# Kernel tuning notes

Hardware: AMD Instinct MI355X
Metric: run time of the kernel (lower is better)

Reference implementation:

```python
import jax, jax.numpy as jnp
import numpy as np

BETA = 0.25
N_EMBED = 1024
DIM = 256


def setup_inputs() -> dict:
    key = jax.random.key(0)
    k1, k2 = jax.random.split(key)
    z = jax.random.normal(k1, (8, DIM, 64, 64), dtype=jnp.float32)
    # matches nn.Embedding init: uniform(-1/n_embed, 1/n_embed)
    codebook = jax.random.uniform(
        k2, (N_EMBED, DIM), dtype=jnp.float32,
        minval=-1.0 / N_EMBED, maxval=1.0 / N_EMBED)
    return {"z": z, "codebook": codebook}


def reference(z, codebook):
    B, C, H, W = z.shape
    sg = jax.lax.stop_gradient
    zp = jnp.transpose(z, (0, 2, 3, 1))          # [B,H,W,C]
    zf = zp.reshape(-1, C)                        # [N,C], N = B*H*W
    # squared euclidean distances: ||z||^2 + ||e||^2 - 2 z.e
    d = (jnp.sum(zf * zf, axis=1, keepdims=True)
         + jnp.sum(codebook * codebook, axis=1)
         - 2.0 * zf @ codebook.T)                 # [N, n_embed]
    idx = jnp.argmin(d, axis=1)                   # [N]
    # one-hot @ codebook in the original is just an index gather
    z_q = codebook[idx].reshape(zp.shape)         # [B,H,W,C]
    loss = (BETA * jnp.mean((sg(z_q) - zp) ** 2)
            + jnp.mean((z_q - sg(zp)) ** 2))
    z_q_st = zp + sg(z_q - zp)                    # straight-through estimator
    z_q_out = jnp.transpose(z_q_st, (0, 3, 1, 2))  # back to NCHW
    return z_q_out, loss, idx.reshape(B, H, W)
```

## Files before the change

kernel.cpp:

```cpp
#include <hip/hip_runtime.h>
#include <hip/hip_fp16.h>

#define NELEM 8388608
#define M_GAP 6e-4f
#define SCORE_SCALE (-1.0f / 512.0f)

typedef _Float16 f16x8 __attribute__((ext_vector_type(8)));
typedef short s16x8 __attribute__((ext_vector_type(8)));
typedef float f32x4 __attribute__((ext_vector_type(4)));

__device__ __forceinline__ unsigned short bf16r(float f) {
  unsigned u = __float_as_uint(f);
  return (unsigned short)((u + 0x7fffu + ((u >> 16) & 1u)) >> 16);
}
__device__ __forceinline__ float bf16f(unsigned short h) {
  return __uint_as_float(((unsigned)h) << 16);
}

__device__ __forceinline__ float pw128_sq(const float* p, int s) {
  float r[8];
#pragma unroll
  for (int j = 0; j < 8; ++j) { float v = p[j * s]; r[j] = __fmul_rn(v, v); }
#pragma unroll
  for (int i = 8; i < 128; i += 8) {
#pragma unroll
    for (int j = 0; j < 8; ++j) {
      float v = p[(i + j) * s];
      r[j] = __fadd_rn(r[j], __fmul_rn(v, v));
    }
  }
  return __fadd_rn(__fadd_rn(__fadd_rn(r[0], r[1]), __fadd_rn(r[2], r[3])),
                   __fadd_rn(__fadd_rn(r[4], r[5]), __fadd_rn(r[6], r[7])));
}
__device__ __forceinline__ float np_sumsq256(const float* p, int s) {
  return __fadd_rn(pw128_sq(p, s), pw128_sq(p + 128 * s, s));
}

__global__ __launch_bounds__(256)
void vq_prep(const float* __restrict__ cb, unsigned short* __restrict__ cbimg,
             float* __restrict__ cbT, float* __restrict__ Bsg,
             unsigned* __restrict__ cnt, float* __restrict__ loss) {
  int gid = blockIdx.x * 256 + threadIdx.x;
  if (gid == 0) { *cnt = 0u; *loss = 0.0f; }
  int j = gid >> 2, qt = gid & 3;
  const float4* row4 = reinterpret_cast<const float4*>(cb + (size_t)j * 256 + qt * 64);
  int jt = j >> 5, jj = j & 31;
  unsigned short* baseh = cbimg + (size_t)jt * 8192 + jj * 256;
  int sw = jj << 3;
#pragma unroll
  for (int m = 0; m < 8; ++m) {
    int c0 = qt * 64 + m * 8;
    float4 va = row4[m * 2];
    float4 vb = row4[m * 2 + 1];
    float v[8] = {va.x, va.y, va.z, va.w, vb.x, vb.y, vb.z, vb.w};
    s16x8 hv;
#pragma unroll
    for (int q = 0; q < 8; ++q) {
      hv[q] = (short)__half_as_ushort(__float2half(v[q] * 1024.0f));
      cbT[(size_t)(c0 + q) * 1024 + j] = v[q];
    }
    *reinterpret_cast<s16x8*>(baseh + (c0 ^ sw)) = hv;
  }
  if (qt == 0) Bsg[j] = np_sumsq256(cb + (size_t)j * 256, 1);
}

__global__ __launch_bounds__(256, 4)
void vq_fast(const float* __restrict__ z, const float* __restrict__ cb,
             const unsigned short* __restrict__ cbimg,
             const float* __restrict__ Bsg,
             float* __restrict__ zq, float* __restrict__ loss,
             float* __restrict__ idxo,
             unsigned* __restrict__ list, unsigned* __restrict__ cnt,
             float* __restrict__ zdump) {
  __shared__ __align__(16) unsigned char buf[34816];
  __shared__ float BsL[1024];
  __shared__ float part[32][36];
  __shared__ float rowA[64];
  __shared__ int bestj[64];
  __shared__ float bestd[64];
  __shared__ unsigned char flg[64];
  __shared__ float wred[4];

  const int t = threadIdx.x;
  const int bid = blockIdx.x;
  const int lane = t & 63;
  const int wv = t >> 6;
  const int l15 = lane & 15;
  const int lk = lane >> 4;

  float* zt = reinterpret_cast<float*>(buf);
  const float4* z4 = reinterpret_cast<const float4*>(
      z + (size_t)(bid >> 6) * 1048576 + (size_t)(bid & 63) * 64);

  f16x8 ah[8];
  for (int hp = 0; hp < 2; ++hp) {
    float sq[4] = {0.f, 0.f, 0.f, 0.f};
#pragma unroll
    for (int i = 0; i < 8; ++i) {
      int idx = t + i * 256;
      int c = idx >> 3, w4p = idx & 7;
      float4 v = z4[(size_t)c * 1024 + hp * 8 + w4p];
      zt[c * 33 + w4p * 4 + 0] = v.x;
      zt[c * 33 + w4p * 4 + 1] = v.y;
      zt[c * 33 + w4p * 4 + 2] = v.z;
      zt[c * 33 + w4p * 4 + 3] = v.w;
      sq[0] += v.x * v.x; sq[1] += v.y * v.y;
      sq[2] += v.z * v.z; sq[3] += v.w * v.w;
    }
#pragma unroll
    for (int q = 0; q < 4; ++q) part[t >> 3][(t & 7) * 4 + q] = sq[q];
    __syncthreads();
    if (t < 32) {
      float s = 0.f;
#pragma unroll
      for (int g = 0; g < 32; ++g) s += part[g][t];
      rowA[hp * 32 + t] = s;
    }
    if ((wv >> 1) == hp) {
      int lr = (wv & 1) * 16 + l15;
#pragma unroll
      for (int kk = 0; kk < 8; ++kk)
#pragma unroll
        for (int m = 0; m < 8; ++m)
          ah[kk][m] = (_Float16)zt[(kk * 32 + lk * 8 + m) * 33 + lr];
    }
    if (zdump) {
#pragma unroll
      for (int i = 0; i < 8; ++i) {
        int item = t + i * 256;
        int c4 = item & 63, rowp = item >> 6;
        float4 v = make_float4(zt[(c4 * 4 + 0) * 33 + rowp],
                               zt[(c4 * 4 + 1) * 33 + rowp],
                               zt[(c4 * 4 + 2) * 33 + rowp],
                               zt[(c4 * 4 + 3) * 33 + rowp]);
        *reinterpret_cast<float4*>(
            zdump + ((size_t)bid * 64 + hp * 32 + rowp) * 256 + c4 * 4) = v;
      }
    }
    __syncthreads();
  }

#pragma unroll
  for (int i = 0; i < 4; ++i) {
    int item = t + i * 256;
    *reinterpret_cast<s16x8*>(buf + item * 16) =
        *reinterpret_cast<const s16x8*>((const unsigned char*)cbimg + item * 16);
  }
  for (int i = t; i < 1024; i += 256) BsL[i] = Bsg[i];
  __syncthreads();

  float b1v[2][4], b2v[2][4];
  int b1i[2][4];
#pragma unroll
  for (int js = 0; js < 2; ++js)
#pragma unroll
    for (int r = 0; r < 4; ++r) { b1v[js][r] = 3.4e38f; b2v[js][r] = 3.4e38f; b1i[js][r] = 0; }

  for (int jt = 0; jt < 32; ++jt) {
    const unsigned short* bufH = reinterpret_cast<const unsigned short*>(buf + (jt & 1) * 16384);
    unsigned char* nbuf = buf + ((jt + 1) & 1) * 16384;
    const unsigned char* nsrc = (const unsigned char*)cbimg + (size_t)(jt + 1) * 16384;

    f32x4 acc[2];
    acc[0] = (f32x4){0.f, 0.f, 0.f, 0.f};
    acc[1] = (f32x4){0.f, 0.f, 0.f, 0.f};

    s16x8 g0, g1, g2, g3;
#pragma unroll
    for (int kk = 0; kk < 8; ++kk) {
      if (jt < 31 && kk == 0) {
        g0 = *reinterpret_cast<const s16x8*>(nsrc + (t + 0) * 16);
        g1 = *reinterpret_cast<const s16x8*>(nsrc + (t + 256) * 16);
        g2 = *reinterpret_cast<const s16x8*>(nsrc + (t + 512) * 16);
        g3 = *reinterpret_cast<const s16x8*>(nsrc + (t + 768) * 16);
      }
#pragma unroll
      for (int js = 0; js < 2; ++js) {
        int jj = js * 16 + l15;
        int e = jj * 256 + ((kk * 32 + lk * 8) ^ (jj << 3));
        f16x8 bh = *reinterpret_cast<const f16x8*>(bufH + e);
        acc[js] = __builtin_amdgcn_mfma_f32_16x16x32_f16(ah[kk], bh, acc[js], 0, 0, 0);
      }
      if (jt < 31 && kk == 4) {
        *reinterpret_cast<s16x8*>(nbuf + (t + 0) * 16) = g0;
        *reinterpret_cast<s16x8*>(nbuf + (t + 256) * 16) = g1;
        *reinterpret_cast<s16x8*>(nbuf + (t + 512) * 16) = g2;
        *reinterpret_cast<s16x8*>(nbuf + (t + 768) * 16) = g3;
      }
    }

#pragma unroll
    for (int js = 0; js < 2; ++js) {
      int j = jt * 32 + js * 16 + l15;
      float Bj = BsL[j];
#pragma unroll
      for (int r = 0; r < 4; ++r) {
        float s = fmaf(SCORE_SCALE, acc[js][r], Bj);
        bool lt = s < b1v[js][r];
        float other = lt ? b1v[js][r] : s;
        b2v[js][r] = fminf(b2v[js][r], other);
        b1v[js][r] = fminf(b1v[js][r], s);
        b1i[js][r] = lt ? j : b1i[js][r];
      }
    }
    __syncthreads();
  }

#pragma unroll
  for (int r = 0; r < 4; ++r) {
    float v1 = b1v[1][r];
    bool lt = v1 < b1v[0][r];
    float hi = lt ? b1v[0][r] : v1;
    b2v[0][r] = fminf(fminf(b2v[0][r], b2v[1][r]), hi);
    b1v[0][r] = fminf(b1v[0][r], v1);
    b1i[0][r] = lt ? b1i[1][r] : b1i[0][r];
  }
#pragma unroll
  for (int mk = 1; mk < 16; mk <<= 1) {
#pragma unroll
    for (int r = 0; r < 4; ++r) {
      float ov1 = __shfl_xor(b1v[0][r], mk, 64);
      float ov2 = __shfl_xor(b2v[0][r], mk, 64);
      int oi1 = __shfl_xor(b1i[0][r], mk, 64);
      bool lt = ov1 < b1v[0][r];
      float hi = lt ? b1v[0][r] : ov1;
      b2v[0][r] = fminf(fminf(b2v[0][r], ov2), hi);
      b1v[0][r] = fminf(b1v[0][r], ov1);
      b1i[0][r] = lt ? oi1 : b1i[0][r];
    }
  }
  if (l15 == 0) {
#pragma unroll
    for (int r = 0; r < 4; ++r) {
      int rr = wv * 16 + lk * 4 + r;
      bestj[rr] = b1i[0][r];
      bestd[rr] = b1v[0][r];
      flg[rr] = (b2v[0][r] - b1v[0][r] <= M_GAP) ? 1 : 0;
    }
  }
  __syncthreads();

  if (t < 64) {
    int n = bid * 64 + t;
    idxo[n] = (float)bestj[t];
    if (flg[t]) { unsigned pos = atomicAdd(cnt, 1u); list[pos] = (unsigned)n; }
  }

  {
    float lv = (t < 64) ? (rowA[t] + bestd[t]) : 0.f;
#pragma unroll
    for (int off = 32; off > 0; off >>= 1) lv += __shfl_down(lv, off, 64);
    if (lane == 0) wred[wv] = lv;
  }
  __syncthreads();
  if (t == 0)
    atomicAdd(loss, (wred[0] + wred[1] + wred[2] + wred[3]) * (1.25f / (float)NELEM));

  f32x4* ldsF4 = reinterpret_cast<f32x4*>(buf);
  const float* ldsF = reinterpret_cast<const float*>(buf);
  const float4* cb4 = reinterpret_cast<const float4*>(cb);
  float* zqb = zq + (size_t)(bid >> 6) * 1048576 + (size_t)(bid & 63) * 64;
  for (int hp = 0; hp < 2; ++hp) {
    __syncthreads();
#pragma unroll
    for (int i = 0; i < 8; ++i) {
      int item = t + i * 256;
      int rr = item >> 6, cc = item & 63;
      float4 v = cb4[(size_t)bestj[hp * 32 + rr] * 64 + cc];
      ldsF4[rr * 64 + (cc ^ ((rr >> 2) & 7))] = (f32x4){v.x, v.y, v.z, v.w};
    }
    __syncthreads();
#pragma unroll
    for (int i = 0; i < 8; ++i) {
      int item = t + i * 256;
      int w4p = item & 7, c = item >> 3;
      float ov[4];
#pragma unroll
      for (int q = 0; q < 4; ++q) {
        int rr = w4p * 4 + q;
        ov[q] = ldsF[(rr * 64 + ((c >> 2) ^ ((rr >> 2) & 7))) * 4 + (c & 3)];
      }
      *reinterpret_cast<float4*>(zqb + (size_t)c * 4096 + hp * 32 + w4p * 4) =
          make_float4(ov[0], ov[1], ov[2], ov[3]);
    }
  }
}

__global__ __launch_bounds__(256)
void vq_exact_fast(const float* __restrict__ zdump, const float* __restrict__ cbT,
                   const float* __restrict__ Bsg, const unsigned* __restrict__ list,
                   const unsigned* __restrict__ cnt, float* __restrict__ idxo) {
  __shared__ float zr[8][260];
  __shared__ float Anp[8];
  __shared__ float rv[256];
  __shared__ int ri[256];
  const int t = threadIdx.x;
  const unsigned K = *cnt;
  const float4* cbT4 = reinterpret_cast<const float4*>(cbT);
  const float4* zd4 = reinterpret_cast<const float4*>(zdump);

  for (unsigned g = blockIdx.x; g * 8 < K; g += gridDim.x) {
    int nrows = (int)min(8u, K - g * 8);
    __syncthreads();
#pragma unroll
    for (int i = 0; i < 2; ++i) {
      int idx = t + i * 256;
      int r = idx >> 6, c4 = idx & 63;
      if (r < nrows) {
        float4 v = zd4[(size_t)list[g * 8 + r] * 64 + c4];
        zr[r][c4 * 4 + 0] = v.x; zr[r][c4 * 4 + 1] = v.y;
        zr[r][c4 * 4 + 2] = v.z; zr[r][c4 * 4 + 3] = v.w;
      }
    }
    __syncthreads();
    if (t < nrows) Anp[t] = np_sumsq256(&zr[t][0], 1);
    __syncthreads();

    float acc[8][4];
#pragma unroll
    for (int r = 0; r < 8; ++r)
#pragma unroll
      for (int q = 0; q < 4; ++q) acc[r][q] = 0.f;
    for (int c = 0; c < 256; ++c) {
      float4 bv = cbT4[c * 256 + t];
#pragma unroll
      for (int r = 0; r < 8; ++r) {
        float zc = zr[r][c];
        acc[r][0] = fmaf(zc, bv.x, acc[r][0]);
        acc[r][1] = fmaf(zc, bv.y, acc[r][1]);
        acc[r][2] = fmaf(zc, bv.z, acc[r][2]);
        acc[r][3] = fmaf(zc, bv.w, acc[r][3]);
      }
    }
    for (int r = 0; r < nrows; ++r) {
      float A = Anp[r];
      float bvv = 3.4e38f;
      int bii = 0;
#pragma unroll
      for (int q = 0; q < 4; ++q) {
        int j = t * 4 + q;
        float dd = __fsub_rn(__fadd_rn(A, Bsg[j]), __fmul_rn(2.0f, acc[r][q]));
        if (dd < bvv) { bvv = dd; bii = j; }
      }
      rv[t] = bvv; ri[t] = bii;
      __syncthreads();
      for (int s2 = 128; s2 > 0; s2 >>= 1) {
        if (t < s2) {
          float v2 = rv[t + s2]; int i2 = ri[t + s2];
          if (v2 < rv[t] || (v2 == rv[t] && i2 < ri[t])) { rv[t] = v2; ri[t] = i2; }
        }
        __syncthreads();
      }
      if (t == 0) idxo[list[g * 8 + r]] = (float)ri[0];
      __syncthreads();
    }
  }
}

__global__ __launch_bounds__(256)
void vq_exact_scatter(const float* __restrict__ z, const float* __restrict__ cbT,
                      const float* __restrict__ Bsg, const unsigned* __restrict__ list,
                      const unsigned* __restrict__ cnt, float* __restrict__ idxo) {
  __shared__ float zr[8][260];
  __shared__ float Anp[8];
  __shared__ float rv[256];
  __shared__ int ri[256];
  const int t = threadIdx.x;
  const unsigned K = *cnt;
  const float4* cbT4 = reinterpret_cast<const float4*>(cbT);

  for (unsigned g = blockIdx.x; g * 8 < K; g += gridDim.x) {
    int nrows = (int)min(8u, K - g * 8);
    __syncthreads();
    {
      int r = t >> 5, l32 = t & 31;
      if (r < nrows) {
        int n = (int)list[g * 8 + r];
        int b = n >> 12, hw = n & 4095;
        const float* zb = z + (size_t)b * 1048576 + hw;
#pragma unroll
        for (int q = 0; q < 8; ++q) {
          int c = l32 * 8 + q;
          zr[r][c] = zb[(size_t)c * 4096];
        }
      }
    }
    __syncthreads();
    if (t < nrows) Anp[t] = np_sumsq256(&zr[t][0], 1);
    __syncthreads();
    float acc[8][4];
#pragma unroll
    for (int r = 0; r < 8; ++r)
#pragma unroll
      for (int q = 0; q < 4; ++q) acc[r][q] = 0.f;
    for (int c = 0; c < 256; ++c) {
      float4 bv = cbT4[c * 256 + t];
#pragma unroll
      for (int r = 0; r < 8; ++r) {
        float zc = zr[r][c];
        acc[r][0] = fmaf(zc, bv.x, acc[r][0]);
        acc[r][1] = fmaf(zc, bv.y, acc[r][1]);
        acc[r][2] = fmaf(zc, bv.z, acc[r][2]);
        acc[r][3] = fmaf(zc, bv.w, acc[r][3]);
      }
    }
    for (int r = 0; r < nrows; ++r) {
      float A = Anp[r];
      float bvv = 3.4e38f;
      int bii = 0;
#pragma unroll
      for (int q = 0; q < 4; ++q) {
        int j = t * 4 + q;
        float dd = __fsub_rn(__fadd_rn(A, Bsg[j]), __fmul_rn(2.0f, acc[r][q]));
        if (dd < bvv) { bvv = dd; bii = j; }
      }
      rv[t] = bvv; ri[t] = bii;
      __syncthreads();
      for (int s2 = 128; s2 > 0; s2 >>= 1) {
        if (t < s2) {
          float v2 = rv[t + s2]; int i2 = ri[t + s2];
          if (v2 < rv[t] || (v2 == rv[t] && i2 < ri[t])) { rv[t] = v2; ri[t] = i2; }
        }
        __syncthreads();
      }
      if (t == 0) idxo[list[g * 8 + r]] = (float)ri[0];
      __syncthreads();
    }
  }
}

__global__ __launch_bounds__(256)
void vq_ref(const float* __restrict__ z, const float* __restrict__ cb,
            float* __restrict__ zq, float* __restrict__ loss,
            float* __restrict__ idxo) {
  __shared__ __align__(16) float zt[256 * 64];
  __shared__ __align__(16) float cbt[256 * 64];
  __shared__ float As[64];
  __shared__ float Bs[64];
  __shared__ int bestj[64];
  __shared__ float cand_v[16 * 64];
  __shared__ int cand_i[16 * 64];
  __shared__ double wred[4];
  const int t = threadIdx.x;
  const int wg = t & 15, jg = t >> 4;
  const int bid = blockIdx.x;
  const int b = bid >> 6, h = bid & 63;
  const int n0 = bid * 64;
  const float4* z4 = reinterpret_cast<const float4*>(z + (size_t)b * 256 * 4096 + (size_t)h * 64);
  float4* zt4 = reinterpret_cast<float4*>(zt);
#pragma unroll
  for (int i = 0; i < 16; ++i) {
    int idx4 = t + i * 256;
    zt4[idx4] = z4[(size_t)(idx4 >> 4) * 1024 + (idx4 & 15)];
  }
  __syncthreads();
  if (t < 64) As[t] = np_sumsq256(zt + t, 64);
  float bv[4]; int bi[4];
#pragma unroll
  for (int a = 0; a < 4; ++a) { bv[a] = 3.4e38f; bi[a] = 0; }
  for (int p = 0; p < 16; ++p) {
    __syncthreads();
    const float4* cb4 = reinterpret_cast<const float4*>(cb) + (size_t)p * 64 * 64;
#pragma unroll
    for (int i = 0; i < 16; ++i) {
      int idx4 = t + i * 256;
      int jj = idx4 >> 6, c4 = idx4 & 63;
      float4 v = cb4[idx4];
      cbt[(c4 * 4 + 0) * 64 + jj] = v.x;
      cbt[(c4 * 4 + 1) * 64 + jj] = v.y;
      cbt[(c4 * 4 + 2) * 64 + jj] = v.z;
      cbt[(c4 * 4 + 3) * 64 + jj] = v.w;
    }
    __syncthreads();
    if (t < 64) Bs[t] = np_sumsq256(cbt + t, 64);
    float acc[4][4];
#pragma unroll
    for (int a = 0; a < 4; ++a)
#pragma unroll
      for (int u = 0; u < 4; ++u) acc[a][u] = 0.0f;
    const float4* ztp = reinterpret_cast<const float4*>(zt) + wg;
    const float4* cbp = reinterpret_cast<const float4*>(cbt) + jg;
#pragma unroll 4
    for (int c = 0; c < 256; ++c) {
      float4 zv = ztp[c * 16];
      float4 cv = cbp[c * 16];
      float za[4] = {zv.x, zv.y, zv.z, zv.w};
      float ca[4] = {cv.x, cv.y, cv.z, cv.w};
#pragma unroll
      for (int a = 0; a < 4; ++a)
#pragma unroll
        for (int u = 0; u < 4; ++u) acc[a][u] = fmaf(za[a], ca[u], acc[a][u]);
    }
    __syncthreads();
#pragma unroll
    for (int u = 0; u < 4; ++u) {
      int j = p * 64 + jg * 4 + u;
      float Bju = Bs[jg * 4 + u];
#pragma unroll
      for (int a = 0; a < 4; ++a) {
        float AB = __fadd_rn(As[wg * 4 + a], Bju);
        float dd = __fsub_rn(AB, __fmul_rn(2.0f, acc[a][u]));
        if (dd < bv[a]) { bv[a] = dd; bi[a] = j; }
      }
    }
  }
  __syncthreads();
#pragma unroll
  for (int a = 0; a < 4; ++a) {
    int w = wg * 4 + a;
    cand_v[jg * 64 + w] = bv[a];
    cand_i[jg * 64 + w] = bi[a];
  }
  __syncthreads();
  if (t < 64) {
    float v0 = cand_v[t]; int i0 = cand_i[t];
    for (int g = 1; g < 16; ++g) {
      float v = cand_v[g * 64 + t]; int ii = cand_i[g * 64 + t];
      if (v < v0 || (v == v0 && ii < i0)) { v0 = v; i0 = ii; }
    }
    bestj[t] = i0;
    idxo[n0 + t] = (float)i0;
  }
  __syncthreads();
  double lsum = 0.0;
  float* zqbase = zq + (size_t)b * 256 * 4096 + (size_t)h * 64;
  for (int i = 0; i < 64; ++i) {
    int idx = t + i * 256;
    int c = idx >> 6, w = idx & 63;
    float zvv = zt[c * 64 + w];
    float cvv = cb[(size_t)bestj[w] * 256 + c];
    zqbase[(size_t)c * 4096 + w] = cvv;
    double d = (double)cvv - (double)zvv;
    lsum += d * d;
  }
#pragma unroll
  for (int off = 32; off > 0; off >>= 1) lsum += __shfl_down(lsum, off, 64);
  if ((t & 63) == 0) wred[t >> 6] = lsum;
  __syncthreads();
  if (t == 0) {
    double tot = wred[0] + wred[1] + wred[2] + wred[3];
    atomicAdd(loss, (float)(tot * (1.25 / (double)NELEM)));
  }
}

extern "C" void kernel_launch(void* const* d_in, const int* in_sizes, int n_in,
                              void* d_out, int out_size, void* d_ws, size_t ws_size,
                              hipStream_t stream) {
  (void)in_sizes; (void)n_in; (void)out_size;
  const float* z = (const float*)d_in[0];
  const float* cb = (const float*)d_in[1];
  float* out = (float*)d_out;
  float* zq = out;
  float* loss = out + NELEM;
  float* idxo = out + NELEM + 1;
  if (ws_size < 1712128) {
    hipMemsetAsync(loss, 0, sizeof(float), stream);
    vq_ref<<<512, 256, 0, stream>>>(z, cb, zq, loss, idxo);
    return;
  }
  unsigned char* ws = (unsigned char*)d_ws;
  unsigned* cnt = (unsigned*)ws;
  float* Bsg = (float*)(ws + 1024);
  unsigned* list = (unsigned*)(ws + 8192);
  float* cbT = (float*)(ws + 139264);
  unsigned short* cbimg = (unsigned short*)(ws + 1187840);
  const bool have_dump = (ws_size >= 35651584);
  float* zdump = have_dump ? (float*)(ws + 2097152) : nullptr;
  vq_prep<<<16, 256, 0, stream>>>(cb, cbimg, cbT, Bsg, cnt, loss);
  vq_fast<<<512, 256, 0, stream>>>(z, cb, cbimg, Bsg, zq, loss, idxo, list, cnt, zdump);
  if (have_dump)
    vq_exact_fast<<<512, 256, 0, stream>>>(zdump, cbT, Bsg, list, cnt, idxo);
  else
    vq_exact_scatter<<<512, 256, 0, stream>>>(z, cbT, Bsg, list, cnt, idxo);
}
```

Measured before the change: 100.2 us.

## Split codebook across waves so each wave scores all 64 rows against its quarter

Each wave now owns a 256-entry slice of the codebook and computes all 64 rows against it, holding four A-fragment sets in registers. This lets each LDS B-fragment read feed four MFMAs instead of one. The codebook image layout changes to 16-row tiles, and per-wave top-2 results are merged through shared memory at the end. The cost is much higher register pressure (launch bounds drop to 2 blocks per CU) and two barriers per iteration instead of one.

```diff
diff --git a/kernel.cpp b/kernel.cpp
--- a/kernel.cpp
+++ b/kernel.cpp
@@ -44,8 +44,8 @@
   if (gid == 0) { *cnt = 0u; *loss = 0.0f; }
   int j = gid >> 2, qt = gid & 3;
   const float4* row4 = reinterpret_cast<const float4*>(cb + (size_t)j * 256 + qt * 64);
-  int jt = j >> 5, jj = j & 31;
-  unsigned short* baseh = cbimg + (size_t)jt * 8192 + jj * 256;
+  int T = j >> 4, jj = j & 15;
+  unsigned short* baseh = cbimg + (size_t)T * 4096 + jj * 256;
   int sw = jj << 3;
 #pragma unroll
   for (int m = 0; m < 8; ++m) {
@@ -64,7 +64,7 @@
   if (qt == 0) Bsg[j] = np_sumsq256(cb + (size_t)j * 256, 1);
 }
 
-__global__ __launch_bounds__(256, 4)
+__global__ __launch_bounds__(256, 2)
 void vq_fast(const float* __restrict__ z, const float* __restrict__ cb,
              const unsigned short* __restrict__ cbimg,
              const float* __restrict__ Bsg,
@@ -80,6 +80,8 @@
   __shared__ float bestd[64];
   __shared__ unsigned char flg[64];
   __shared__ float wred[4];
+  __shared__ float cv1[4 * 64], cv2[4 * 64];
+  __shared__ int ci1[4 * 64];
 
   const int t = threadIdx.x;
   const int bid = blockIdx.x;
@@ -92,7 +94,7 @@
   const float4* z4 = reinterpret_cast<const float4*>(
       z + (size_t)(bid >> 6) * 1048576 + (size_t)(bid & 63) * 64);
 
-  f16x8 ah[8];
+  f16x8 ah[4][8];
   for (int hp = 0; hp < 2; ++hp) {
     float sq[4] = {0.f, 0.f, 0.f, 0.f};
 #pragma unroll
@@ -116,13 +118,15 @@
       for (int g = 0; g < 32; ++g) s += part[g][t];
       rowA[hp * 32 + t] = s;
     }
-    if ((wv >> 1) == hp) {
-      int lr = (wv & 1) * 16 + l15;
+#pragma unroll
+    for (int rr2 = 0; rr2 < 2; ++rr2) {
+      int rs = hp * 2 + rr2;
+      int lr = rr2 * 16 + l15;
 #pragma unroll
       for (int kk = 0; kk < 8; ++kk)
 #pragma unroll
         for (int m = 0; m < 8; ++m)
-          ah[kk][m] = (_Float16)zt[(kk * 32 + lk * 8 + m) * 33 + lr];
+          ah[rs][kk][m] = (_Float16)zt[(kk * 32 + lk * 8 + m) * 33 + lr];
     }
     if (zdump) {
 #pragma unroll
@@ -140,111 +144,117 @@
     __syncthreads();
   }
 
-#pragma unroll
-  for (int i = 0; i < 4; ++i) {
-    int item = t + i * 256;
-    *reinterpret_cast<s16x8*>(buf + item * 16) =
-        *reinterpret_cast<const s16x8*>((const unsigned char*)cbimg + item * 16);
+  s16x8* sbuf = reinterpret_cast<s16x8*>(buf);
+  const s16x8* cimg = reinterpret_cast<const s16x8*>(cbimg);
+#pragma unroll
+  for (int i = 0; i < 8; ++i) {
+    int gidx = t + i * 256;
+    sbuf[gidx] = cimg[(size_t)((gidx >> 9) * 16 + 0) * 512 + (gidx & 511)];
   }
   for (int i = t; i < 1024; i += 256) BsL[i] = Bsg[i];
   __syncthreads();
 
-  float b1v[2][4], b2v[2][4];
-  int b1i[2][4];
-#pragma unroll
-  for (int js = 0; js < 2; ++js)
-#pragma unroll
-    for (int r = 0; r < 4; ++r) { b1v[js][r] = 3.4e38f; b2v[js][r] = 3.4e38f; b1i[js][r] = 0; }
-
-  for (int jt = 0; jt < 32; ++jt) {
-    const unsigned short* bufH = reinterpret_cast<const unsigned short*>(buf + (jt & 1) * 16384);
-    unsigned char* nbuf = buf + ((jt + 1) & 1) * 16384;
-    const unsigned char* nsrc = (const unsigned char*)cbimg + (size_t)(jt + 1) * 16384;
-
-    f32x4 acc[2];
-    acc[0] = (f32x4){0.f, 0.f, 0.f, 0.f};
-    acc[1] = (f32x4){0.f, 0.f, 0.f, 0.f};
-
-    s16x8 g0, g1, g2, g3;
+  float b1v[4][4], b2v[4][4];
+  int b1i[4][4];
+#pragma unroll
+  for (int rs = 0; rs < 4; ++rs)
+#pragma unroll
+    for (int r = 0; r < 4; ++r) { b1v[rs][r] = 3.4e38f; b2v[rs][r] = 3.4e38f; b1i[rs][r] = 0; }
+
+  const unsigned short* wbuf = reinterpret_cast<const unsigned short*>(buf) + wv * 4096;
+
+  for (int it = 0; it < 16; ++it) {
+    s16x8 g[8];
+    if (it < 15) {
+#pragma unroll
+      for (int i = 0; i < 8; ++i) {
+        int gidx = t + i * 256;
+        g[i] = cimg[(size_t)((gidx >> 9) * 16 + it + 1) * 512 + (gidx & 511)];
+      }
+    }
+
+    f32x4 acc[4];
+#pragma unroll
+    for (int rs = 0; rs < 4; ++rs) acc[rs] = (f32x4){0.f, 0.f, 0.f, 0.f};
 #pragma unroll
     for (int kk = 0; kk < 8; ++kk) {
-      if (jt < 31 && kk == 0) {
-        g0 = *reinterpret_cast<const s16x8*>(nsrc + (t + 0) * 16);
-        g1 = *reinterpret_cast<const s16x8*>(nsrc + (t + 256) * 16);
-        g2 = *reinterpret_cast<const s16x8*>(nsrc + (t + 512) * 16);
-        g3 = *reinterpret_cast<const s16x8*>(nsrc + (t + 768) * 16);
-      }
-#pragma unroll
-      for (int js = 0; js < 2; ++js) {
-        int jj = js * 16 + l15;
-        int e = jj * 256 + ((kk * 32 + lk * 8) ^ (jj << 3));
-        f16x8 bh = *reinterpret_cast<const f16x8*>(bufH + e);
-        acc[js] = __builtin_amdgcn_mfma_f32_16x16x32_f16(ah[kk], bh, acc[js], 0, 0, 0);
-      }
-      if (jt < 31 && kk == 4) {
-        *reinterpret_cast<s16x8*>(nbuf + (t + 0) * 16) = g0;
-        *reinterpret_cast<s16x8*>(nbuf + (t + 256) * 16) = g1;
-        *reinterpret_cast<s16x8*>(nbuf + (t + 512) * 16) = g2;
-        *reinterpret_cast<s16x8*>(nbuf + (t + 768) * 16) = g3;
-      }
-    }
-
-#pragma unroll
-    for (int js = 0; js < 2; ++js) {
-      int j = jt * 32 + js * 16 + l15;
+      int e = l15 * 256 + ((kk * 32 + lk * 8) ^ (l15 << 3));
+      f16x8 bh = *reinterpret_cast<const f16x8*>(wbuf + e);
+#pragma unroll
+      for (int rs = 0; rs < 4; ++rs)
+        acc[rs] = __builtin_amdgcn_mfma_f32_16x16x32_f16(ah[rs][kk], bh, acc[rs], 0, 0, 0);
+    }
+
+    {
+      int j = wv * 256 + it * 16 + l15;
       float Bj = BsL[j];
 #pragma unroll
+      for (int rs = 0; rs < 4; ++rs)
+#pragma unroll
+        for (int r = 0; r < 4; ++r) {
+          float s = fmaf(SCORE_SCALE, acc[rs][r], Bj);
+          bool lt = s < b1v[rs][r];
+          float other = lt ? b1v[rs][r] : s;
+          b2v[rs][r] = fminf(b2v[rs][r], other);
+          b1v[rs][r] = fminf(b1v[rs][r], s);
+          b1i[rs][r] = lt ? j : b1i[rs][r];
+        }
+    }
+    __syncthreads();
+    if (it < 15) {
+#pragma unroll
+      for (int i = 0; i < 8; ++i) sbuf[t + i * 256] = g[i];
+    }
+    __syncthreads();
+  }
+
+#pragma unroll
+  for (int mk = 1; mk < 16; mk <<= 1) {
+#pragma unroll
+    for (int rs = 0; rs < 4; ++rs)
+#pragma unroll
       for (int r = 0; r < 4; ++r) {
-        float s = fmaf(SCORE_SCALE, acc[js][r], Bj);
-        bool lt = s < b1v[js][r];
-        float other = lt ? b1v[js][r] : s;
-        b2v[js][r] = fminf(b2v[js][r], other);
-        b1v[js][r] = fminf(b1v[js][r], s);
-        b1i[js][r] = lt ? j : b1i[js][r];
-      }
-    }
-    __syncthreads();
-  }
-
-#pragma unroll
-  for (int r = 0; r < 4; ++r) {
-    float v1 = b1v[1][r];
-    bool lt = v1 < b1v[0][r];
-    float hi = lt ? b1v[0][r] : v1;
-    b2v[0][r] = fminf(fminf(b2v[0][r], b2v[1][r]), hi);
-    b1v[0][r] = fminf(b1v[0][r], v1);
-    b1i[0][r] = lt ? b1i[1][r] : b1i[0][r];
-  }
-#pragma unroll
-  for (int mk = 1; mk < 16; mk <<= 1) {
-#pragma unroll
-    for (int r = 0; r < 4; ++r) {
-      float ov1 = __shfl_xor(b1v[0][r], mk, 64);
-      float ov2 = __shfl_xor(b2v[0][r], mk, 64);
-      int oi1 = __shfl_xor(b1i[0][r], mk, 64);
-      bool lt = ov1 < b1v[0][r];
-      float hi = lt ? b1v[0][r] : ov1;
-      b2v[0][r] = fminf(fminf(b2v[0][r], ov2), hi);
-      b1v[0][r] = fminf(b1v[0][r], ov1);
-      b1i[0][r] = lt ? oi1 : b1i[0][r];
-    }
+        float ov1 = __shfl_xor(b1v[rs][r], mk, 64);
+        float ov2 = __shfl_xor(b2v[rs][r], mk, 64);
+        int oi1 = __shfl_xor(b1i[rs][r], mk, 64);
+        bool lt = ov1 < b1v[rs][r];
+        float hi = lt ? b1v[rs][r] : ov1;
+        b2v[rs][r] = fminf(fminf(b2v[rs][r], ov2), hi);
+        b1v[rs][r] = fminf(b1v[rs][r], ov1);
+        b1i[rs][r] = lt ? oi1 : b1i[rs][r];
+      }
   }
   if (l15 == 0) {
 #pragma unroll
-    for (int r = 0; r < 4; ++r) {
-      int rr = wv * 16 + lk * 4 + r;
-      bestj[rr] = b1i[0][r];
-      bestd[rr] = b1v[0][r];
-      flg[rr] = (b2v[0][r] - b1v[0][r] <= M_GAP) ? 1 : 0;
-    }
+    for (int rs = 0; rs < 4; ++rs)
+#pragma unroll
+      for (int r = 0; r < 4; ++r) {
+        int rr = rs * 16 + lk * 4 + r;
+        cv1[wv * 64 + rr] = b1v[rs][r];
+        cv2[wv * 64 + rr] = b2v[rs][r];
+        ci1[wv * 64 + rr] = b1i[rs][r];
+      }
   }
   __syncthreads();
 
   if (t < 64) {
+    float v1 = cv1[t], v2 = cv2[t];
+    int i1 = ci1[t];
+#pragma unroll
+    for (int w = 1; w < 4; ++w) {
+      float u1 = cv1[w * 64 + t], u2 = cv2[w * 64 + t];
+      int ui = ci1[w * 64 + t];
+      if (u1 < v1) { v2 = fminf(v1, u2); v1 = u1; i1 = ui; }
+      else v2 = fminf(v2, u1);
+    }
+    bestj[t] = i1;
+    bestd[t] = v1;
+    flg[t] = (v2 - v1 <= M_GAP) ? 1 : 0;
     int n = bid * 64 + t;
-    idxo[n] = (float)bestj[t];
+    idxo[n] = (float)i1;
     if (flg[t]) { unsigned pos = atomicAdd(cnt, 1u); list[pos] = (unsigned)n; }
   }
+  __syncthreads();
 
   {
     float lv = (t < 64) ? (rowA[t] + bestd[t]) : 0.f;
```

Result: slower. 103.6 us (+3.4%).
